# Kernel tuning notes

Measured on AMD Instinct MI355X. Metric: run time of the kernel, lower is better.

The kernel has to match this reference:

```python
import jax, jax.numpy as jnp
import numpy as np

D, H, C = 128, 256, 10
SEQ, BATCH = 2048, 64


def _lstm_layer(x, Wih, Whh, b):
    """PyTorch-style LSTM layer. x: [S,B,Din], Wih: [4H,Din], Whh: [4H,H], b: [4H].
    Gate order i,f,g,o. Returns hidden sequence [S,B,H]."""
    # precompute input projections for all timesteps at once
    xw = jnp.einsum('sbd,gd->sbg', x, Wih) + b  # [S,B,4H]
    h0 = jnp.zeros((x.shape[1], Whh.shape[1]), x.dtype)
    c0 = jnp.zeros_like(h0)

    def step(carry, xw_t):
        h, c = carry
        gates = xw_t + h @ Whh.T  # [B,4H]
        i, f, g, o = jnp.split(gates, 4, axis=-1)
        i = jax.nn.sigmoid(i)
        f = jax.nn.sigmoid(f)
        g = jnp.tanh(g)
        o = jax.nn.sigmoid(o)
        c = f * c + i * g
        h = o * jnp.tanh(c)
        return (h, c), h

    _, hs = jax.lax.scan(step, (h0, c0), xw)
    return hs  # [S,B,H]


def setup_inputs() -> dict:
    key = jax.random.key(0)
    ks = jax.random.split(key, 8)
    s1 = 1.0 / np.sqrt(H)
    x = jax.random.normal(ks[0], (SEQ, BATCH, D), jnp.float32)
    Wih1 = jax.random.uniform(ks[1], (4 * H, D), jnp.float32, -s1, s1)
    Whh1 = jax.random.uniform(ks[2], (4 * H, H), jnp.float32, -s1, s1)
    b1 = jax.random.uniform(ks[3], (4 * H,), jnp.float32, -s1, s1)  # b_ih + b_hh folded
    Wih2 = jax.random.uniform(ks[4], (4 * H, H), jnp.float32, -s1, s1)
    Whh2 = jax.random.uniform(ks[5], (4 * H, H), jnp.float32, -s1, s1)
    b2 = jax.random.uniform(ks[6], (4 * H,), jnp.float32, -s1, s1)
    Wlin = jax.random.uniform(ks[7], (C, H), jnp.float32, -s1, s1)
    blin = jnp.zeros((C,), jnp.float32)
    return {"x": x, "Wih1": Wih1, "Whh1": Whh1, "b1": b1,
            "Wih2": Wih2, "Whh2": Whh2, "b2": b2,
            "Wlin": Wlin, "blin": blin}


def reference(x, Wih1, Whh1, b1, Wih2, Whh2, b2, Wlin, blin):
    h1 = jnp.tanh(_lstm_layer(x, Wih1, Whh1, b1))          # [S,B,H]
    h2 = jnp.tanh(_lstm_layer(h1, Wih2, Whh2, b2))         # [S,B,H]
    # squeeze() is a no-op for S>1, B>1
    out = jax.nn.sigmoid(jnp.einsum('sbh,ch->sbc', h2, Wlin) + blin)  # [S,B,C]
    return out
```

## Files before the change

### kernel.cpp

```cpp
#include <hip/hip_runtime.h>

typedef _Float16 half8 __attribute__((ext_vector_type(8)));
typedef float    f32x4 __attribute__((ext_vector_type(4)));

static constexpr int S_ = 2048;
static constexpr int B_ = 64;
static constexpr int D_ = 128;
static constexpr int H_ = 256;
static constexpr int C_ = 10;

static constexpr int NBLK = 64;
static constexpr int NTHR = 512;
static constexpr int HHALF = B_ * H_;

__device__ __attribute__((aligned(64))) unsigned g_f[NBLK * 16];

#define LD_AG(p)    __hip_atomic_load((p), __ATOMIC_RELAXED, __HIP_MEMORY_SCOPE_AGENT)
#define ST_AG(p, v) __hip_atomic_store((p), (v), __ATOMIC_RELAXED, __HIP_MEMORY_SCOPE_AGENT)

__device__ __forceinline__ float fs(float v) { return 1.0f / (1.0f + __expf(-v)); }
__device__ __forceinline__ float ft(float v) { return 1.0f - 2.0f / (__expf(2.0f * v) + 1.0f); }

__device__ __forceinline__ half8 ldh16(const _Float16* p) {
    union { double d[2]; half8 h; } u;
    u.d[0] = LD_AG((const double*)p);
    u.d[1] = LD_AG(((const double*)p) + 1);
    return u.h;
}

__device__ __forceinline__ void ldg16x8(half8* r,
    const _Float16* p0, const _Float16* p1, const _Float16* p2, const _Float16* p3,
    const _Float16* p4, const _Float16* p5, const _Float16* p6, const _Float16* p7)
{
    asm volatile(
        "global_load_dwordx4 %0, %8, off sc0 sc1\n\t"
        "global_load_dwordx4 %1, %9, off sc0 sc1\n\t"
        "global_load_dwordx4 %2, %10, off sc0 sc1\n\t"
        "global_load_dwordx4 %3, %11, off sc0 sc1\n\t"
        "global_load_dwordx4 %4, %12, off sc0 sc1\n\t"
        "global_load_dwordx4 %5, %13, off sc0 sc1\n\t"
        "global_load_dwordx4 %6, %14, off sc0 sc1\n\t"
        "global_load_dwordx4 %7, %15, off sc0 sc1\n\t"
        "s_waitcnt vmcnt(0)"
        : "=&v"(r[0]), "=&v"(r[1]), "=&v"(r[2]), "=&v"(r[3]),
          "=&v"(r[4]), "=&v"(r[5]), "=&v"(r[6]), "=&v"(r[7])
        : "v"(p0), "v"(p1), "v"(p2), "v"(p3),
          "v"(p4), "v"(p5), "v"(p6), "v"(p7)
        : "memory");
}

__device__ __forceinline__ half8 cvt8(float4 a, float4 b) {
    half8 r;
    r[0] = (_Float16)a.x; r[1] = (_Float16)a.y; r[2] = (_Float16)a.z; r[3] = (_Float16)a.w;
    r[4] = (_Float16)b.x; r[5] = (_Float16)b.y; r[6] = (_Float16)b.z; r[7] = (_Float16)b.w;
    return r;
}

__global__ __launch_bounds__(NTHR, 1)
void lstm2_ef(const float* __restrict__ x,
              const float* __restrict__ Wih1, const float* __restrict__ Whh1,
              const float* __restrict__ b1,
              const float* __restrict__ Wih2, const float* __restrict__ Whh2,
              const float* __restrict__ b2,
              const float* __restrict__ Wlin, const float* __restrict__ blin,
              float* __restrict__ out, _Float16* __restrict__ hb)
{
    const int bid = blockIdx.x, tid = threadIdx.x;
    const bool isL2 = (bid >= 32);
    const int blk  = bid & 31;
    const int lane = tid & 63, w = tid >> 6;
    const int mt   = w & 3;
    const int nt   = w >> 2;
    const int n    = lane & 15;
    const int kg   = lane >> 4;
    const int c4   = n >> 2, gate = n & 3;
    const int lc   = nt * 4 + c4;
    const int col  = blk * 8 + lc;
    const int rowg = gate * H_ + col;
    const int batchA = mt * 16 + n;

    _Float16* h1raw = hb;
    _Float16* h1t   = hb + 3 * HHALF;
    _Float16* h2raw = hb + 6 * HHALF;
    _Float16* h2t   = hb + 9 * HHALF;

    __shared__ __align__(16) _Float16 sh[2][B_][8];

    const unsigned base = LD_AG(&g_f[bid * 16]);

    { double* z = (double*)hb;
      for (int i = bid * NTHR + tid; i < 49152; i += NBLK * NTHR) ST_AG(z + i, 0.0); }

    half8 bfrag[16];
    if (!isL2) {
        #pragma unroll
        for (int kt = 0; kt < 4; ++kt) {
            const float* p = Wih1 + (size_t)rowg * D_ + kt * 32 + kg * 8;
            bfrag[kt] = cvt8(*(const float4*)p, *(const float4*)(p + 4));
        }
        #pragma unroll
        for (int kt = 4; kt < 12; ++kt) {
            const float* p = Whh1 + (size_t)rowg * H_ + (kt - 4) * 32 + kg * 8;
            bfrag[kt] = cvt8(*(const float4*)p, *(const float4*)(p + 4));
        }
    } else {
        #pragma unroll
        for (int kt = 0; kt < 8; ++kt) {
            const float* p = Wih2 + (size_t)rowg * H_ + kt * 32 + kg * 8;
            bfrag[kt] = cvt8(*(const float4*)p, *(const float4*)(p + 4));
        }
        #pragma unroll
        for (int kt = 8; kt < 16; ++kt) {
            const float* p = Whh2 + (size_t)rowg * H_ + (kt - 8) * 32 + kg * 8;
            bfrag[kt] = cvt8(*(const float4*)p, *(const float4*)(p + 4));
        }
    }
    const float bias_n = isL2 ? b2[rowg] : b1[rowg];

    __syncthreads();
    if (tid == 0) ST_AG(&g_f[bid * 16], base + 1u);

    float cr[4] = {0.f, 0.f, 0.f, 0.f};

    float4 xf0, xf1, xf2, xf3;
    if (!isL2) {
        const float* xr = x + (size_t)batchA * D_;
        xf0 = *(const float4*)(xr + (kg * 8));
        xf1 = *(const float4*)(xr + (32 + kg * 8));
        xf2 = *(const float4*)(xr + (64 + kg * 8));
        xf3 = *(const float4*)(xr + (96 + kg * 8));
    }

    int w3 = 0;

    for (int t = 0; t <= S_ + 1; ++t) {
        const int r1 = (w3 == 0) ? 2 : w3 - 1;
        const int r2 = (w3 == 2) ? 0 : w3 + 1;

        {
            const unsigned et1 = base + (unsigned)t + 1u;
            if (tid < 64) {
                const unsigned tg = (tid < 32 || isL2 || t == 0) ? et1 : et1 - 1u;
                while ((int)(LD_AG(&g_f[tid * 16]) - tg) < 0) {}
            }
            __syncthreads();
        }

        if (!isL2) {
            if (t < S_) {
                half8 af[12];
                {
                    const float* xr = x + ((size_t)t * B_ + batchA) * D_;
                    af[0] = cvt8(xf0, *(const float4*)(xr + (kg * 8) + 4));
                    af[1] = cvt8(xf1, *(const float4*)(xr + (32 + kg * 8) + 4));
                    af[2] = cvt8(xf2, *(const float4*)(xr + (64 + kg * 8) + 4));
                    af[3] = cvt8(xf3, *(const float4*)(xr + (96 + kg * 8) + 4));
                }
                const _Float16* hp = h1raw + r1 * HHALF + (((size_t)kg * 64 + batchA) << 3);
                ldg16x8(&af[4], hp,          hp + 2048,  hp + 4096,  hp + 6144,
                                hp + 8192,   hp + 10240, hp + 12288, hp + 14336);
                f32x4 accA = {0.f, 0.f, 0.f, 0.f}, accB = {0.f, 0.f, 0.f, 0.f};
                #pragma unroll
                for (int kt = 0; kt < 12; kt += 2) {
                    accA = __builtin_amdgcn_mfma_f32_16x16x32_f16(af[kt],     bfrag[kt],     accA, 0, 0, 0);
                    accB = __builtin_amdgcn_mfma_f32_16x16x32_f16(af[kt + 1], bfrag[kt + 1], accB, 0, 0, 0);
                }
                #pragma unroll
                for (int r = 0; r < 4; ++r) {
                    const float pre = accA[r] + accB[r] + bias_n;
                    const float av  = (gate == 2) ? ft(pre) : fs(pre);
                    const int lb = (lane & 48) | (c4 << 2);
                    const float gi = __shfl(av, lb | 0, 64), gf = __shfl(av, lb | 1, 64);
                    const float gg = __shfl(av, lb | 2, 64), go = __shfl(av, lb | 3, 64);
                    const float cn = gf * cr[r] + gi * gg; cr[r] = cn;
                    const float hv = go * ft(cn);
                    const int bD = mt * 16 + kg * 4 + r;
                    if (gate == 0) sh[0][bD][lc] = (_Float16)hv;
                    if (gate == 1) sh[1][bD][lc] = (_Float16)ft(hv);
                }
            }
        } else {
            if (t >= 1 && t <= S_) {
                half8 af[16];
                const _Float16* h1p = h1t   + r1 * HHALF + (((size_t)kg * 64 + batchA) << 3);
                const _Float16* h2p = h2raw + r2 * HHALF + (((size_t)kg * 64 + batchA) << 3);
                ldg16x8(&af[0], h1p,         h1p + 2048,  h1p + 4096,  h1p + 6144,
                                h1p + 8192,  h1p + 10240, h1p + 12288, h1p + 14336);
                ldg16x8(&af[8], h2p,         h2p + 2048,  h2p + 4096,  h2p + 6144,
                                h2p + 8192,  h2p + 10240, h2p + 12288, h2p + 14336);
                f32x4 accA = {0.f, 0.f, 0.f, 0.f}, accB = {0.f, 0.f, 0.f, 0.f};
                #pragma unroll
                for (int kt = 0; kt < 16; kt += 2) {
                    accA = __builtin_amdgcn_mfma_f32_16x16x32_f16(af[kt],     bfrag[kt],     accA, 0, 0, 0);
                    accB = __builtin_amdgcn_mfma_f32_16x16x32_f16(af[kt + 1], bfrag[kt + 1], accB, 0, 0, 0);
                }
                #pragma unroll
                for (int r = 0; r < 4; ++r) {
                    const float pre = accA[r] + accB[r] + bias_n;
                    const float av  = (gate == 2) ? ft(pre) : fs(pre);
                    const int lb = (lane & 48) | (c4 << 2);
                    const float gi = __shfl(av, lb | 0, 64), gf = __shfl(av, lb | 1, 64);
                    const float gg = __shfl(av, lb | 2, 64), go = __shfl(av, lb | 3, 64);
                    const float cn = gf * cr[r] + gi * gg; cr[r] = cn;
                    const float hv = go * ft(cn);
                    const int bD = mt * 16 + kg * 4 + r;
                    if (gate == 0) sh[0][bD][lc] = (_Float16)hv;
                    if (gate == 1) sh[1][bD][lc] = (_Float16)ft(hv);
                }
            }
        }

        __syncthreads();

        if (tid < 64) {
            const int b = tid;
            bool doit; int slot;
            if (!isL2) { doit = (t < S_);            slot = w3; }
            else       { doit = (t >= 1 && t <= S_); slot = r1; }
            if (doit) {
                const double* s0 = (const double*)&sh[0][b][0];
                const double* s1 = (const double*)&sh[1][b][0];
                _Float16* braw = isL2 ? h2raw : h1raw;
                _Float16* btnh = isL2 ? h2t   : h1t;
                double* d0 = (double*)(braw + slot * HHALF + ((blk * 64 + b) << 3));
                double* d1 = (double*)(btnh + slot * HHALF + ((blk * 64 + b) << 3));
                ST_AG(d0, s0[0]); ST_AG(d0 + 1, s0[1]);
                ST_AG(d1, s1[0]); ST_AG(d1 + 1, s1[1]);
            }
            asm volatile("s_waitcnt vmcnt(0)" ::: "memory");
            __builtin_amdgcn_sched_barrier(0);
            if (tid == 0) ST_AG(&g_f[bid * 16], base + (unsigned)t + 2u);
        }

        if (!isL2 && t + 1 < S_) {
            const float* xr = x + ((size_t)(t + 1) * B_ + batchA) * D_;
            xf0 = *(const float4*)(xr + (kg * 8));
            xf1 = *(const float4*)(xr + (32 + kg * 8));
            xf2 = *(const float4*)(xr + (64 + kg * 8));
            xf3 = *(const float4*)(xr + (96 + kg * 8));
        }
        if (isL2 && t >= 2) {
            const int g16 = tid >> 4;
            if (g16 < 20) {
                const int dot = blk * 20 + g16, cls = dot >> 6, ob = dot & 63, l16 = tid & 15;
                const _Float16* hB = h2t + r2 * HHALF;
                const half8 v0 = ldh16(hB + (((2 * l16)     * 64 + ob) << 3));
                const half8 v1 = ldh16(hB + (((2 * l16 + 1) * 64 + ob) << 3));
                const float* wr = Wlin + (size_t)cls * H_ + l16 * 16;
                float p = 0.f;
                #pragma unroll
                for (int j = 0; j < 8; ++j) p += (float)v0[j] * wr[j] + (float)v1[j] * wr[8 + j];
                p += __shfl_xor(p, 1, 64); p += __shfl_xor(p, 2, 64);
                p += __shfl_xor(p, 4, 64); p += __shfl_xor(p, 8, 64);
                if (l16 == 0)
                    out[((size_t)(t - 2) * B_ + ob) * C_ + cls] = fs(p + blin[cls]);
            }
        }

        w3 = r2;
    }
}

extern "C" void kernel_launch(void* const* d_in, const int* in_sizes, int n_in,
                              void* d_out, int out_size, void* d_ws, size_t ws_size,
                              hipStream_t stream)
{
    const float* x    = (const float*)d_in[0];
    const float* Wih1 = (const float*)d_in[1];
    const float* Whh1 = (const float*)d_in[2];
    const float* b1   = (const float*)d_in[3];
    const float* Wih2 = (const float*)d_in[4];
    const float* Whh2 = (const float*)d_in[5];
    const float* b2   = (const float*)d_in[6];
    const float* Wlin = (const float*)d_in[7];
    const float* blin = (const float*)d_in[8];
    float* out = (float*)d_out;
    _Float16* hb = (_Float16*)d_ws;

    void* args[] = { (void*)&x, (void*)&Wih1, (void*)&Whh1, (void*)&b1,
                     (void*)&Wih2, (void*)&Whh2, (void*)&b2,
                     (void*)&Wlin, (void*)&blin, (void*)&out, (void*)&hb };
    hipLaunchCooperativeKernel((const void*)lstm2_ef, dim3(NBLK), dim3(NTHR),
                               args, 0, stream);
}
```

Before: 9.611 ms.

## Stage recurrent hidden-state loads through LDS, shared across N-tile waves

Instead of every wave loading the full h vectors from global memory each timestep, only a subset of waves (nt==0 for layer 1, split by layer input for layer 2) issue the coherent global loads and write them into a shared LDS buffer. The other waves read their A fragments from LDS after an extra barrier. The per-step h stores are also merged from paired 8-byte atomic stores into single 16-byte coherent stores. This cuts redundant L2 traffic on the latency-critical recurrent path, at the cost of an extra __syncthreads and LDS round trip per step.

```diff
diff --git a/kernel.cpp b/kernel.cpp
--- a/kernel.cpp
+++ b/kernel.cpp
@@ -47,6 +47,11 @@
         : "v"(p0), "v"(p1), "v"(p2), "v"(p3),
           "v"(p4), "v"(p5), "v"(p6), "v"(p7)
         : "memory");
+}
+
+__device__ __forceinline__ void stg16(_Float16* p, half8 v) {
+    asm volatile("global_store_dwordx4 %0, %1, off sc0 sc1"
+                 :: "v"(p), "v"(v) : "memory");
 }
 
 __device__ __forceinline__ half8 cvt8(float4 a, float4 b) {
@@ -85,6 +90,7 @@
     _Float16* h2t   = hb + 9 * HHALF;
 
     __shared__ __align__(16) _Float16 sh[2][B_][8];
+    __shared__ __align__(16) half8 stga[64][64];
 
     const unsigned base = LD_AG(&g_f[bid * 16]);
 
@@ -145,6 +151,36 @@
             }
             __syncthreads();
         }
+
+        if (!isL2) {
+            if (nt == 0 && t < S_) {
+                const _Float16* hp = h1raw + r1 * HHALF + (((size_t)kg * 64 + batchA) << 3);
+                half8 tmp[8];
+                ldg16x8(tmp, hp,          hp + 2048,  hp + 4096,  hp + 6144,
+                             hp + 8192,   hp + 10240, hp + 12288, hp + 14336);
+                #pragma unroll
+                for (int kt = 0; kt < 8; ++kt) stga[kt * 4 + mt][lane] = tmp[kt];
+            }
+        } else {
+            if (t >= 1 && t <= S_) {
+                if (nt == 0) {
+                    const _Float16* h1p = h1t + r1 * HHALF + (((size_t)kg * 64 + batchA) << 3);
+                    half8 tmp[8];
+                    ldg16x8(tmp, h1p,         h1p + 2048,  h1p + 4096,  h1p + 6144,
+                                 h1p + 8192,  h1p + 10240, h1p + 12288, h1p + 14336);
+                    #pragma unroll
+                    for (int kt = 0; kt < 8; ++kt) stga[kt * 4 + mt][lane] = tmp[kt];
+                } else {
+                    const _Float16* h2p = h2raw + r2 * HHALF + (((size_t)kg * 64 + batchA) << 3);
+                    half8 tmp[8];
+                    ldg16x8(tmp, h2p,         h2p + 2048,  h2p + 4096,  h2p + 6144,
+                                 h2p + 8192,  h2p + 10240, h2p + 12288, h2p + 14336);
+                    #pragma unroll
+                    for (int kt = 0; kt < 8; ++kt) stga[32 + kt * 4 + mt][lane] = tmp[kt];
+                }
+            }
+        }
+        __syncthreads();
 
         if (!isL2) {
             if (t < S_) {
@@ -156,9 +192,8 @@
                     af[2] = cvt8(xf2, *(const float4*)(xr + (64 + kg * 8) + 4));
                     af[3] = cvt8(xf3, *(const float4*)(xr + (96 + kg * 8) + 4));
                 }
-                const _Float16* hp = h1raw + r1 * HHALF + (((size_t)kg * 64 + batchA) << 3);
-                ldg16x8(&af[4], hp,          hp + 2048,  hp + 4096,  hp + 6144,
-                                hp + 8192,   hp + 10240, hp + 12288, hp + 14336);
+                #pragma unroll
+                for (int kt = 0; kt < 8; ++kt) af[4 + kt] = stga[kt * 4 + mt][lane];
                 f32x4 accA = {0.f, 0.f, 0.f, 0.f}, accB = {0.f, 0.f, 0.f, 0.f};
                 #pragma unroll
                 for (int kt = 0; kt < 12; kt += 2) {
@@ -182,12 +217,10 @@
         } else {
             if (t >= 1 && t <= S_) {
                 half8 af[16];
-                const _Float16* h1p = h1t   + r1 * HHALF + (((size_t)kg * 64 + batchA) << 3);
-                const _Float16* h2p = h2raw + r2 * HHALF + (((size_t)kg * 64 + batchA) << 3);
-                ldg16x8(&af[0], h1p,         h1p + 2048,  h1p + 4096,  h1p + 6144,
-                                h1p + 8192,  h1p + 10240, h1p + 12288, h1p + 14336);
-                ldg16x8(&af[8], h2p,         h2p + 2048,  h2p + 4096,  h2p + 6144,
-                                h2p + 8192,  h2p + 10240, h2p + 12288, h2p + 14336);
+                #pragma unroll
+                for (int kt = 0; kt < 8; ++kt) af[kt]     = stga[kt * 4 + mt][lane];
+                #pragma unroll
+                for (int kt = 0; kt < 8; ++kt) af[8 + kt] = stga[32 + kt * 4 + mt][lane];
                 f32x4 accA = {0.f, 0.f, 0.f, 0.f}, accB = {0.f, 0.f, 0.f, 0.f};
                 #pragma unroll
                 for (int kt = 0; kt < 16; kt += 2) {
@@ -218,14 +251,12 @@
             if (!isL2) { doit = (t < S_);            slot = w3; }
             else       { doit = (t >= 1 && t <= S_); slot = r1; }
             if (doit) {
-                const double* s0 = (const double*)&sh[0][b][0];
-                const double* s1 = (const double*)&sh[1][b][0];
+                const half8 s0 = *(const half8*)&sh[0][b][0];
+                const half8 s1 = *(const half8*)&sh[1][b][0];
                 _Float16* braw = isL2 ? h2raw : h1raw;
                 _Float16* btnh = isL2 ? h2t   : h1t;
-                double* d0 = (double*)(braw + slot * HHALF + ((blk * 64 + b) << 3));
-                double* d1 = (double*)(btnh + slot * HHALF + ((blk * 64 + b) << 3));
-                ST_AG(d0, s0[0]); ST_AG(d0 + 1, s0[1]);
-                ST_AG(d1, s1[0]); ST_AG(d1 + 1, s1[1]);
+                stg16(braw + slot * HHALF + ((blk * 64 + b) << 3), s0);
+                stg16(btnh + slot * HHALF + ((blk * 64 + b) << 3), s1);
             }
             asm volatile("s_waitcnt vmcnt(0)" ::: "memory");
             __builtin_amdgcn_sched_barrier(0);
```

Measured after the change: 10.08 ms. 1.05x slower.

## Split batch into two independent halves with separate flags to pipeline LSTM steps

Applied to the files above, without the earlier changes.

Halves the block to 256 threads and processes the 64-batch as two 32-row halves in sequence within each timestep. Each half has its own grid sync flag, so one half's cross-block wait can overlap with the other half's compute. The h stores are also merged into one 16-byte store per thread. In exchange, each wave does twice as many sequential phases per step, with extra syncthreads and flag traffic, and only half as many waves are active.

```diff
diff --git a/kernel.cpp b/kernel.cpp
--- a/kernel.cpp
+++ b/kernel.cpp
@@ -10,10 +10,10 @@
 static constexpr int C_ = 10;
 
 static constexpr int NBLK = 64;
-static constexpr int NTHR = 512;
+static constexpr int NTHR = 256;
 static constexpr int HHALF = B_ * H_;
 
-__device__ __attribute__((aligned(64))) unsigned g_f[NBLK * 16];
+__device__ __attribute__((aligned(64))) unsigned g_f[NBLK * 2 * 16];
 
 #define LD_AG(p)    __hip_atomic_load((p), __ATOMIC_RELAXED, __HIP_MEMORY_SCOPE_AGENT)
 #define ST_AG(p, v) __hip_atomic_store((p), (v), __ATOMIC_RELAXED, __HIP_MEMORY_SCOPE_AGENT)
@@ -49,6 +49,11 @@
         : "memory");
 }
 
+__device__ __forceinline__ void stg16(_Float16* p, half8 v) {
+    asm volatile("global_store_dwordx4 %0, %1, off sc0 sc1"
+                 :: "v"(p), "v"(v) : "memory");
+}
+
 __device__ __forceinline__ half8 cvt8(float4 a, float4 b) {
     half8 r;
     r[0] = (_Float16)a.x; r[1] = (_Float16)a.y; r[2] = (_Float16)a.z; r[3] = (_Float16)a.w;
@@ -56,8 +61,122 @@
     return r;
 }
 
+#define PIPE_BODY(P, BASEP, BAP, CRP, XFP)                                          \
+    {                                                                               \
+        const unsigned et1 = (BASEP) + (unsigned)t + 1u;                            \
+        if (tid < 64) {                                                             \
+            const unsigned tg = (tid < 32 || isL2 || t == 0) ? et1 : et1 - 1u;      \
+            while ((int)(LD_AG(&g_f[(tid * 2 + (P)) * 16]) - tg) < 0) {}            \
+        }                                                                           \
+        __syncthreads();                                                            \
+        if (!isL2) {                                                                \
+            if (t < S_) {                                                           \
+                half8 af[12];                                                       \
+                const float* xr = x + ((size_t)t * B_ + (BAP)) * D_;                \
+                af[0] = cvt8(XFP[0], *(const float4*)(xr + (kg * 8) + 4));          \
+                af[1] = cvt8(XFP[1], *(const float4*)(xr + (32 + kg * 8) + 4));     \
+                af[2] = cvt8(XFP[2], *(const float4*)(xr + (64 + kg * 8) + 4));     \
+                af[3] = cvt8(XFP[3], *(const float4*)(xr + (96 + kg * 8) + 4));     \
+                const _Float16* hp = h1raw + r1 * HHALF + (((size_t)kg * 64 + (BAP)) << 3); \
+                ldg16x8(&af[4], hp,          hp + 2048,  hp + 4096,  hp + 6144,     \
+                                hp + 8192,   hp + 10240, hp + 12288, hp + 14336);   \
+                f32x4 accA = {0.f, 0.f, 0.f, 0.f}, accB = {0.f, 0.f, 0.f, 0.f};     \
+                _Pragma("unroll")                                                   \
+                for (int kt = 0; kt < 12; kt += 2) {                                \
+                    accA = __builtin_amdgcn_mfma_f32_16x16x32_f16(af[kt],     bfrag[kt],     accA, 0, 0, 0); \
+                    accB = __builtin_amdgcn_mfma_f32_16x16x32_f16(af[kt + 1], bfrag[kt + 1], accB, 0, 0, 0); \
+                }                                                                   \
+                _Pragma("unroll")                                                   \
+                for (int r = 0; r < 4; ++r) {                                       \
+                    const float pre = accA[r] + accB[r] + bias_n;                   \
+                    const float av  = (gate == 2) ? ft(pre) : fs(pre);              \
+                    const int lb = (lane & 48) | (c4 << 2);                         \
+                    const float gi = __shfl(av, lb | 0, 64), gf = __shfl(av, lb | 1, 64); \
+                    const float gg = __shfl(av, lb | 2, 64), go = __shfl(av, lb | 3, 64); \
+                    const float cn = gf * CRP[r] + gi * gg; CRP[r] = cn;            \
+                    const float hv = go * ft(cn);                                   \
+                    const int bD = (P) * 32 + m2 * 16 + kg * 4 + r;                 \
+                    if (gate == 0) sh[0][bD][lc] = (_Float16)hv;                    \
+                    if (gate == 1) sh[1][bD][lc] = (_Float16)ft(hv);                \
+                }                                                                   \
+            }                                                                       \
+        } else {                                                                    \
+            if (t >= 1 && t <= S_) {                                                \
+                half8 af[16];                                                       \
+                const _Float16* h1p = h1t   + r1 * HHALF + (((size_t)kg * 64 + (BAP)) << 3); \
+                const _Float16* h2p = h2raw + r2 * HHALF + (((size_t)kg * 64 + (BAP)) << 3); \
+                ldg16x8(&af[0], h1p,         h1p + 2048,  h1p + 4096,  h1p + 6144,  \
+                                h1p + 8192,  h1p + 10240, h1p + 12288, h1p + 14336);\
+                ldg16x8(&af[8], h2p,         h2p + 2048,  h2p + 4096,  h2p + 6144,  \
+                                h2p + 8192,  h2p + 10240, h2p + 12288, h2p + 14336);\
+                f32x4 accA = {0.f, 0.f, 0.f, 0.f}, accB = {0.f, 0.f, 0.f, 0.f};     \
+                _Pragma("unroll")                                                   \
+                for (int kt = 0; kt < 16; kt += 2) {                                \
+                    accA = __builtin_amdgcn_mfma_f32_16x16x32_f16(af[kt],     bfrag[kt],     accA, 0, 0, 0); \
+                    accB = __builtin_amdgcn_mfma_f32_16x16x32_f16(af[kt + 1], bfrag[kt + 1], accB, 0, 0, 0); \
+                }                                                                   \
+                _Pragma("unroll")                                                   \
+                for (int r = 0; r < 4; ++r) {                                       \
+                    const float pre = accA[r] + accB[r] + bias_n;                   \
+                    const float av  = (gate == 2) ? ft(pre) : fs(pre);              \
+                    const int lb = (lane & 48) | (c4 << 2);                         \
+                    const float gi = __shfl(av, lb | 0, 64), gf = __shfl(av, lb | 1, 64); \
+                    const float gg = __shfl(av, lb | 2, 64), go = __shfl(av, lb | 3, 64); \
+                    const float cn = gf * CRP[r] + gi * gg; CRP[r] = cn;            \
+                    const float hv = go * ft(cn);                                   \
+                    const int bD = (P) * 32 + m2 * 16 + kg * 4 + r;                 \
+                    if (gate == 0) sh[0][bD][lc] = (_Float16)hv;                    \
+                    if (gate == 1) sh[1][bD][lc] = (_Float16)ft(hv);                \
+                }                                                                   \
+            }                                                                       \
+        }                                                                           \
+        __syncthreads();                                     \
+        if (tid < 64) {                                                             \
+            bool doit; int slot;                                                    \
+            if (!isL2) { doit = (t < S_);            slot = w3; }                   \
+            else       { doit = (t >= 1 && t <= S_); slot = r1; }                   \
+            if (doit) {                                                             \
+                const int row = (P) * 32 + (tid & 31);                              \
+                const int buf = tid >> 5;                                           \
+                const half8 s = *(const half8*)&sh[buf][row][0];                    \
+                _Float16* bb = buf ? (isL2 ? h2t : h1t) : (isL2 ? h2raw : h1raw);   \
+                stg16(bb + slot * HHALF + ((blk * 64 + row) << 3), s);              \
+            }                                                                       \
+            asm volatile("s_waitcnt vmcnt(0)" ::: "memory");                        \
+            __builtin_amdgcn_sched_barrier(0);                                      \
+            if (tid == 0) ST_AG(&g_f[(bid * 2 + (P)) * 16], (BASEP) + (unsigned)t + 2u); \
+        }                                                                           \
+                                 \
+        if (!isL2 && t + 1 < S_) {                                                  \
+            const float* xr = x + ((size_t)(t + 1) * B_ + (BAP)) * D_;              \
+            XFP[0] = *(const float4*)(xr + (kg * 8));                               \
+            XFP[1] = *(const float4*)(xr + (32 + kg * 8));                          \
+            XFP[2] = *(const float4*)(xr + (64 + kg * 8));                          \
+            XFP[3] = *(const float4*)(xr + (96 + kg * 8));                          \
+        }                                                                           \
+        if (isL2 && t >= 2) {                                                       \
+            const int hg = (tid >> 4) - 4;           \
+            if (hg >= 0 && hg < 10) {                                               \
+                const int dot = blk * 10 + hg, cls = dot >> 5, ob = dot & 31;       \
+                const int l16 = tid & 15;                                           \
+                const int batch = (P) * 32 + ob;                                    \
+                const _Float16* hB = h2t + r2 * HHALF;                              \
+                const half8 v0 = ldh16(hB + (((2 * l16)     * 64 + batch) << 3));   \
+                const half8 v1 = ldh16(hB + (((2 * l16 + 1) * 64 + batch) << 3));   \
+                const float* wr = Wlin + (size_t)cls * H_ + l16 * 16;               \
+                float p = 0.f;                                                      \
+                _Pragma("unroll")                                                   \
+                for (int j = 0; j < 8; ++j) p += (float)v0[j] * wr[j] + (float)v1[j] * wr[8 + j]; \
+                p += __shfl_xor(p, 1, 64); p += __shfl_xor(p, 2, 64);               \
+                p += __shfl_xor(p, 4, 64); p += __shfl_xor(p, 8, 64);               \
+                if (l16 == 0)                                                       \
+                    out[((size_t)(t - 2) * B_ + batch) * C_ + cls] = fs(p + blin[cls]); \
+            }                                                                       \
+        }                                                                           \
+    }
+
 __global__ __launch_bounds__(NTHR, 1)
-void lstm2_ef(const float* __restrict__ x,
+void lstm2_pp(const float* __restrict__ x,
               const float* __restrict__ Wih1, const float* __restrict__ Whh1,
               const float* __restrict__ b1,
               const float* __restrict__ Wih2, const float* __restrict__ Whh2,
@@ -69,15 +188,16 @@
     const bool isL2 = (bid >= 32);
     const int blk  = bid & 31;
     const int lane = tid & 63, w = tid >> 6;
-    const int mt   = w & 3;
-    const int nt   = w >> 2;
+    const int m2   = w & 1;
+    const int nt   = w >> 1;
     const int n    = lane & 15;
     const int kg   = lane >> 4;
     const int c4   = n >> 2, gate = n & 3;
     const int lc   = nt * 4 + c4;
     const int col  = blk * 8 + lc;
     const int rowg = gate * H_ + col;
-    const int batchA = mt * 16 + n;
+    const int bA0  = m2 * 16 + n;
+    const int bA1  = 32 + m2 * 16 + n;
 
     _Float16* h1raw = hb;
     _Float16* h1t   = hb + 3 * HHALF;
@@ -86,7 +206,8 @@
 
     __shared__ __align__(16) _Float16 sh[2][B_][8];
 
-    const unsigned base = LD_AG(&g_f[bid * 16]);
+    const unsigned baseA = LD_AG(&g_f[(bid * 2 + 0) * 16]);
+    const unsigned baseB = LD_AG(&g_f[(bid * 2 + 1) * 16]);
 
     { double* z = (double*)hb;
       for (int i = bid * NTHR + tid; i < 49152; i += NBLK * NTHR) ST_AG(z + i, 0.0); }
@@ -118,17 +239,23 @@
     const float bias_n = isL2 ? b2[rowg] : b1[rowg];
 
     __syncthreads();
-    if (tid == 0) ST_AG(&g_f[bid * 16], base + 1u);
-
-    float cr[4] = {0.f, 0.f, 0.f, 0.f};
-
-    float4 xf0, xf1, xf2, xf3;
+    if (tid == 0) {
+        ST_AG(&g_f[(bid * 2 + 0) * 16], baseA + 1u);
+        ST_AG(&g_f[(bid * 2 + 1) * 16], baseB + 1u);
+    }
+
+    float crA[4] = {0.f, 0.f, 0.f, 0.f};
+    float crB[4] = {0.f, 0.f, 0.f, 0.f};
+
+    float4 xfA[4] = {}, xfB[4] = {};
     if (!isL2) {
-        const float* xr = x + (size_t)batchA * D_;
-        xf0 = *(const float4*)(xr + (kg * 8));
-        xf1 = *(const float4*)(xr + (32 + kg * 8));
-        xf2 = *(const float4*)(xr + (64 + kg * 8));
-        xf3 = *(const float4*)(xr + (96 + kg * 8));
+        const float* xr0 = x + (size_t)bA0 * D_;
+        const float* xr1 = x + (size_t)bA1 * D_;
+        #pragma unroll
+        for (int q = 0; q < 4; ++q) {
+            xfA[q] = *(const float4*)(xr0 + q * 32 + kg * 8);
+            xfB[q] = *(const float4*)(xr1 + q * 32 + kg * 8);
+        }
     }
 
     int w3 = 0;
@@ -137,125 +264,8 @@
         const int r1 = (w3 == 0) ? 2 : w3 - 1;
         const int r2 = (w3 == 2) ? 0 : w3 + 1;
 
-        {
-            const unsigned et1 = base + (unsigned)t + 1u;
-            if (tid < 64) {
-                const unsigned tg = (tid < 32 || isL2 || t == 0) ? et1 : et1 - 1u;
-                while ((int)(LD_AG(&g_f[tid * 16]) - tg) < 0) {}
-            }
-            __syncthreads();
-        }
-
-        if (!isL2) {
-            if (t < S_) {
-                half8 af[12];
-                {
-                    const float* xr = x + ((size_t)t * B_ + batchA) * D_;
-                    af[0] = cvt8(xf0, *(const float4*)(xr + (kg * 8) + 4));
-                    af[1] = cvt8(xf1, *(const float4*)(xr + (32 + kg * 8) + 4));
-                    af[2] = cvt8(xf2, *(const float4*)(xr + (64 + kg * 8) + 4));
-                    af[3] = cvt8(xf3, *(const float4*)(xr + (96 + kg * 8) + 4));
-                }
-                const _Float16* hp = h1raw + r1 * HHALF + (((size_t)kg * 64 + batchA) << 3);
-                ldg16x8(&af[4], hp,          hp + 2048,  hp + 4096,  hp + 6144,
-                                hp + 8192,   hp + 10240, hp + 12288, hp + 14336);
-                f32x4 accA = {0.f, 0.f, 0.f, 0.f}, accB = {0.f, 0.f, 0.f, 0.f};
-                #pragma unroll
-                for (int kt = 0; kt < 12; kt += 2) {
-                    accA = __builtin_amdgcn_mfma_f32_16x16x32_f16(af[kt],     bfrag[kt],     accA, 0, 0, 0);
-                    accB = __builtin_amdgcn_mfma_f32_16x16x32_f16(af[kt + 1], bfrag[kt + 1], accB, 0, 0, 0);
-                }
-                #pragma unroll
-                for (int r = 0; r < 4; ++r) {
-                    const float pre = accA[r] + accB[r] + bias_n;
-                    const float av  = (gate == 2) ? ft(pre) : fs(pre);
-                    const int lb = (lane & 48) | (c4 << 2);
-                    const float gi = __shfl(av, lb | 0, 64), gf = __shfl(av, lb | 1, 64);
-                    const float gg = __shfl(av, lb | 2, 64), go = __shfl(av, lb | 3, 64);
-                    const float cn = gf * cr[r] + gi * gg; cr[r] = cn;
-                    const float hv = go * ft(cn);
-                    const int bD = mt * 16 + kg * 4 + r;
-                    if (gate == 0) sh[0][bD][lc] = (_Float16)hv;
-                    if (gate == 1) sh[1][bD][lc] = (_Float16)ft(hv);
-                }
-            }
-        } else {
-            if (t >= 1 && t <= S_) {
-                half8 af[16];
-                const _Float16* h1p = h1t   + r1 * HHALF + (((size_t)kg * 64 + batchA) << 3);
-                const _Float16* h2p = h2raw + r2 * HHALF + (((size_t)kg * 64 + batchA) << 3);
-                ldg16x8(&af[0], h1p,         h1p + 2048,  h1p + 4096,  h1p + 6144,
-                                h1p + 8192,  h1p + 10240, h1p + 12288, h1p + 14336);
-                ldg16x8(&af[8], h2p,         h2p + 2048,  h2p + 4096,  h2p + 6144,
-                                h2p + 8192,  h2p + 10240, h2p + 12288, h2p + 14336);
-                f32x4 accA = {0.f, 0.f, 0.f, 0.f}, accB = {0.f, 0.f, 0.f, 0.f};
-                #pragma unroll
-                for (int kt = 0; kt < 16; kt += 2) {
-                    accA = __builtin_amdgcn_mfma_f32_16x16x32_f16(af[kt],     bfrag[kt],     accA, 0, 0, 0);
-                    accB = __builtin_amdgcn_mfma_f32_16x16x32_f16(af[kt + 1], bfrag[kt + 1], accB, 0, 0, 0);
-                }
-                #pragma unroll
-                for (int r = 0; r < 4; ++r) {
-                    const float pre = accA[r] + accB[r] + bias_n;
-                    const float av  = (gate == 2) ? ft(pre) : fs(pre);
-                    const int lb = (lane & 48) | (c4 << 2);
-                    const float gi = __shfl(av, lb | 0, 64), gf = __shfl(av, lb | 1, 64);
-                    const float gg = __shfl(av, lb | 2, 64), go = __shfl(av, lb | 3, 64);
-                    const float cn = gf * cr[r] + gi * gg; cr[r] = cn;
-                    const float hv = go * ft(cn);
-                    const int bD = mt * 16 + kg * 4 + r;
-                    if (gate == 0) sh[0][bD][lc] = (_Float16)hv;
-                    if (gate == 1) sh[1][bD][lc] = (_Float16)ft(hv);
-                }
-            }
-        }
-
-        __syncthreads();
-
-        if (tid < 64) {
-            const int b = tid;
-            bool doit; int slot;
-            if (!isL2) { doit = (t < S_);            slot = w3; }
-            else       { doit = (t >= 1 && t <= S_); slot = r1; }
-            if (doit) {
-                const double* s0 = (const double*)&sh[0][b][0];
-                const double* s1 = (const double*)&sh[1][b][0];
-                _Float16* braw = isL2 ? h2raw : h1raw;
-                _Float16* btnh = isL2 ? h2t   : h1t;
-                double* d0 = (double*)(braw + slot * HHALF + ((blk * 64 + b) << 3));
-                double* d1 = (double*)(btnh + slot * HHALF + ((blk * 64 + b) << 3));
-                ST_AG(d0, s0[0]); ST_AG(d0 + 1, s0[1]);
-                ST_AG(d1, s1[0]); ST_AG(d1 + 1, s1[1]);
-            }
-            asm volatile("s_waitcnt vmcnt(0)" ::: "memory");
-            __builtin_amdgcn_sched_barrier(0);
-            if (tid == 0) ST_AG(&g_f[bid * 16], base + (unsigned)t + 2u);
-        }
-
-        if (!isL2 && t + 1 < S_) {
-            const float* xr = x + ((size_t)(t + 1) * B_ + batchA) * D_;
-            xf0 = *(const float4*)(xr + (kg * 8));
-            xf1 = *(const float4*)(xr + (32 + kg * 8));
-            xf2 = *(const float4*)(xr + (64 + kg * 8));
-            xf3 = *(const float4*)(xr + (96 + kg * 8));
-        }
-        if (isL2 && t >= 2) {
-            const int g16 = tid >> 4;
-            if (g16 < 20) {
-                const int dot = blk * 20 + g16, cls = dot >> 6, ob = dot & 63, l16 = tid & 15;
-                const _Float16* hB = h2t + r2 * HHALF;
-                const half8 v0 = ldh16(hB + (((2 * l16)     * 64 + ob) << 3));
-                const half8 v1 = ldh16(hB + (((2 * l16 + 1) * 64 + ob) << 3));
-                const float* wr = Wlin + (size_t)cls * H_ + l16 * 16;
-                float p = 0.f;
-                #pragma unroll
-                for (int j = 0; j < 8; ++j) p += (float)v0[j] * wr[j] + (float)v1[j] * wr[8 + j];
-                p += __shfl_xor(p, 1, 64); p += __shfl_xor(p, 2, 64);
-                p += __shfl_xor(p, 4, 64); p += __shfl_xor(p, 8, 64);
-                if (l16 == 0)
-                    out[((size_t)(t - 2) * B_ + ob) * C_ + cls] = fs(p + blin[cls]);
-            }
-        }
+        PIPE_BODY(0, baseA, bA0, crA, xfA)
+        PIPE_BODY(1, baseB, bA1, crB, xfB)
 
         w3 = r2;
     }
@@ -280,6 +290,6 @@
     void* args[] = { (void*)&x, (void*)&Wih1, (void*)&Whh1, (void*)&b1,
                      (void*)&Wih2, (void*)&Whh2, (void*)&b2,
                      (void*)&Wlin, (void*)&blin, (void*)&out, (void*)&hb };
-    hipLaunchCooperativeKernel((const void*)lstm2_ef, dim3(NBLK), dim3(NTHR),
+    hipLaunchCooperativeKernel((const void*)lstm2_pp, dim3(NBLK), dim3(NTHR),
                                args, 0, stream);
 }
```

After: 15.11 ms. +57.2%, slower.
